# Kernel tuning notes

Measured on AMD Instinct MI355X. Metric: run time of the kernel, lower is better.

## Reference

```python
import jax, jax.numpy as jnp
import numpy as np

D_MODEL = 768
D_STATE = 16
K_CONV = 4
BATCH = 2
SEQ = 2048


def setup_inputs() -> dict:
    key = jax.random.key(0)
    ks = jax.random.split(key, 16)
    dm, ds, K = D_MODEL, D_STATE, K_CONV
    s = 0.02
    inp = {
        "x": jax.random.normal(ks[0], (BATCH, SEQ, dm), dtype=jnp.float32),
        # linear weights stored (in, out); y = x @ W + b (equivalent to torch Linear)
        "Wi": jax.random.normal(ks[1], (dm, 2 * dm), dtype=jnp.float32) * s,
        "bi": jnp.zeros((2 * dm,), jnp.float32),
        "Wconv": jax.random.normal(ks[2], (dm, K), dtype=jnp.float32) * s,
        "bconv": jnp.zeros((dm,), jnp.float32),
        "Wdt": jax.random.normal(ks[3], (dm, dm), dtype=jnp.float32) * s,
        "bdt": jnp.zeros((dm,), jnp.float32),
        "WB": jax.random.normal(ks[4], (dm, dm * ds), dtype=jnp.float32) * s,
        "bB": jnp.zeros((dm * ds,), jnp.float32),
        "WC": jax.random.normal(ks[5], (dm, dm * ds), dtype=jnp.float32) * s,
        "bC": jnp.zeros((dm * ds,), jnp.float32),
        "A_log": jnp.zeros((dm, ds), jnp.float32),  # matches nn.Parameter(torch.zeros)
        "D": jnp.ones((dm,), jnp.float32),          # matches nn.Parameter(torch.ones)
        "Wo": jax.random.normal(ks[6], (dm, dm), dtype=jnp.float32) * s,
        "bo": jnp.zeros((dm,), jnp.float32),
    }
    return inp


def _forward(x, Wi, bi, Wconv, bconv, Wdt, bdt, WB, bB, WC, bC, A_log, D, Wo, bo):
    B, L, dm = x.shape
    ds = A_log.shape[1]
    K = Wconv.shape[1]

    uv = x @ Wi + bi                        # (B, L, 2*dm)
    u, v = uv[..., :dm], uv[..., dm:]

    # causal depthwise conv1d: torch pads K-1 both sides, keeps first L outputs
    u_pad = jnp.pad(u, ((0, 0), (K - 1, 0), (0, 0)))
    u_conv = bconv + sum(u_pad[:, k:k + L, :] * Wconv[:, k] for k in range(K))

    dt = jax.nn.softplus(u_conv @ Wdt + bdt)            # (B, L, dm)
    Bt = (u_conv @ WB + bB).reshape(B, L, dm, ds)       # (B, L, dm, ds)
    Ct = (u_conv @ WC + bC).reshape(B, L, dm, ds)
    A = -jnp.exp(A_log)                                  # (dm, ds)

    def step(s, inputs):
        dt_t, u_t, B_tt, C_tt = inputs                   # (B,dm), (B,dm), (B,dm,ds), (B,dm,ds)
        dt_e = dt_t[..., None]
        s = s * jnp.exp(dt_e * A) + dt_e * B_tt * u_t[..., None]
        y = jnp.sum(C_tt * s, axis=-1) + D * u_t         # (B, dm)
        return s, y

    s0 = jnp.zeros((B, dm, ds), x.dtype)
    xs = (dt.transpose(1, 0, 2), u_conv.transpose(1, 0, 2),
          Bt.transpose(1, 0, 2, 3), Ct.transpose(1, 0, 2, 3))
    _, ys = jax.lax.scan(step, s0, xs)                   # ys: (L, B, dm)
    y = ys.transpose(1, 0, 2)

    y = y * jax.nn.sigmoid(v)
    return y @ Wo + bo


def reference(x, Wi, bi, Wconv, bconv, Wdt, bdt, WB, bB, WC, bC, A_log, D, Wo, bo):
    return _forward(x, Wi, bi, Wconv, bconv, Wdt, bdt, WB, bB, WC, bC, A_log, D, Wo, bo)
```

## Files before the change

kernel.cpp:

```cpp
#include <hip/hip_runtime.h>

#define DM 768
#define DS 16
#define SEQ 2048
#define BATCH 2
#define MROWS (BATCH*SEQ)
#define N_UV (2*DM)
#define N_BC (DM*DS)
#define NGRP (BATCH*DM/4)
#define SWAVES 16

typedef _Float16 half8 __attribute__((ext_vector_type(8)));
typedef float floatx4 __attribute__((ext_vector_type(4)));
typedef int i32x4 __attribute__((ext_vector_type(4)));
typedef unsigned short us8 __attribute__((ext_vector_type(8)));
typedef signed char c8 __attribute__((ext_vector_type(8)));

static __device__ __forceinline__ unsigned short f2h(float f) {
  _Float16 h = (_Float16)f;
  return __builtin_bit_cast(unsigned short, h);
}
static __device__ __forceinline__ float h2f(unsigned short u) {
  return (float)__builtin_bit_cast(_Float16, u);
}
static __device__ __forceinline__ float softplus_f(float x) {
  return (x > 20.f) ? x : log1pf(__expf(x));
}
static __device__ __forceinline__ void async_cp16(const void* g, void* l) {
  __builtin_amdgcn_global_load_lds(
      (const __attribute__((address_space(1))) void*)g,
      (__attribute__((address_space(3))) void*)l, 16, 0, 0);
}
static __device__ __forceinline__ float row_reduce16(float v) {
  int x;
  x = __builtin_amdgcn_update_dpp(0, __builtin_bit_cast(int, v), 0x128, 0xf, 0xf, true);
  v += __builtin_bit_cast(float, x);
  x = __builtin_amdgcn_update_dpp(0, __builtin_bit_cast(int, v), 0x124, 0xf, 0xf, true);
  v += __builtin_bit_cast(float, x);
  x = __builtin_amdgcn_update_dpp(0, __builtin_bit_cast(int, v), 0x122, 0xf, 0xf, true);
  v += __builtin_bit_cast(float, x);
  x = __builtin_amdgcn_update_dpp(0, __builtin_bit_cast(int, v), 0x121, 0xf, 0xf, true);
  v += __builtin_bit_cast(float, x);
  return v;
}

__global__ void convert_f2h(const float* __restrict__ in,
                            unsigned short* __restrict__ out, int n) {
  int i = (blockIdx.x * blockDim.x + threadIdx.x) * 4;
  if (i >= n) return;
  float4 f = *(const float4*)(in + i);
  ushort4 h;
  h.x = f2h(f.x); h.y = f2h(f.y); h.z = f2h(f.z); h.w = f2h(f.w);
  *(ushort4*)(out + i) = h;
}

__global__ void transpose_w5(const float* __restrict__ W0, const float* __restrict__ W1,
                             const float* __restrict__ W2, const float* __restrict__ W3,
                             const float* __restrict__ W4,
                             unsigned short* __restrict__ T0, unsigned short* __restrict__ T1,
                             unsigned short* __restrict__ T2, unsigned short* __restrict__ T3,
                             unsigned short* __restrict__ T4,
                             int N0, int N1, int N2, int N3, int N4) {
  const float* W; unsigned short* WT; int N;
  switch (blockIdx.z) {
    case 0: W = W0; WT = T0; N = N0; break;
    case 1: W = W1; WT = T1; N = N1; break;
    case 2: W = W2; WT = T2; N = N2; break;
    case 3: W = W3; WT = T3; N = N3; break;
    default: W = W4; WT = T4; N = N4; break;
  }
  int n0 = blockIdx.x * 32;
  if (n0 >= N) return;
  int k0 = blockIdx.y * 32;
  __shared__ float tile[32][33];
  int tx = threadIdx.x, ty = threadIdx.y;
#pragma unroll
  for (int i = 0; i < 32; i += 8)
    tile[ty + i][tx] = W[(size_t)(k0 + ty + i) * N + (n0 + tx)];
  __syncthreads();
  int kp = tx & 15, half = tx >> 4;
#pragma unroll
  for (int i = 0; i < 2; i++) {
    int nl = ty + half * 8 + i * 16;
    unsigned int pk = (unsigned int)f2h(tile[2 * kp][nl]) |
                      ((unsigned int)f2h(tile[2 * kp + 1][nl]) << 16);
    *(unsigned int*)&WT[(size_t)(n0 + nl) * DM + k0 + 2 * kp] = pk;
  }
}

__global__ void transpose_act3(const unsigned short* __restrict__ dt,
                               const unsigned short* __restrict__ uc,
                               const unsigned short* __restrict__ uv,
                               unsigned short* __restrict__ dtT,
                               unsigned short* __restrict__ ucT,
                               unsigned short* __restrict__ vT) {
  const unsigned short* src; unsigned short* dst; int ld, coff;
  switch (blockIdx.z) {
    case 0:  src = dt; dst = dtT; ld = DM;   coff = 0;  break;
    case 1:  src = uc; dst = ucT; ld = DM;   coff = 0;  break;
    default: src = uv; dst = vT;  ld = N_UV; coff = DM; break;
  }
  __shared__ unsigned short tile[32][33];
  int r0 = blockIdx.x * 32, c0 = blockIdx.y * 32;
  int tx = threadIdx.x, ty = threadIdx.y;
#pragma unroll
  for (int i = 0; i < 32; i += 8)
    tile[ty + i][tx] = src[(size_t)(r0 + ty + i) * ld + coff + c0 + tx];
  __syncthreads();
#pragma unroll
  for (int i = 0; i < 32; i += 8)
    dst[(size_t)(c0 + ty + i) * MROWS + r0 + tx] = tile[tx][ty + i];
}

__global__ __launch_bounds__(256)
void quant_rows(const unsigned short* __restrict__ in0,
                const unsigned short* __restrict__ in1,
                signed char* __restrict__ out0, signed char* __restrict__ out1,
                float* __restrict__ sc0, float* __restrict__ sc1, int R) {
  const unsigned short* in = blockIdx.y ? in1 : in0;
  signed char* out = blockIdx.y ? out1 : out0;
  float* scp = blockIdx.y ? sc1 : sc0;
  int row = blockIdx.x * 4 + (threadIdx.x >> 6);
  if (row >= R) return;
  int lane = threadIdx.x & 63;
  const us8* ch = (const us8*)(in + (size_t)row * DM);
  us8 a = ch[lane];
  us8 b = ch[64 + (lane & 31)];
  float fa[8], fb[8];
  float m = 0.f;
#pragma unroll
  for (int j = 0; j < 8; j++) { fa[j] = h2f(a[j]); m = fmaxf(m, fabsf(fa[j])); }
#pragma unroll
  for (int j = 0; j < 8; j++) fb[j] = h2f(b[j]);
  if (lane < 32) {
#pragma unroll
    for (int j = 0; j < 8; j++) m = fmaxf(m, fabsf(fb[j]));
  }
#pragma unroll
  for (int off = 32; off; off >>= 1) m = fmaxf(m, __shfl_xor(m, off));
  float inv = (m > 0.f) ? 127.f / m : 0.f;
  if (lane == 0) scp[row] = m * (1.f / 127.f);
  c8 qa, qb;
#pragma unroll
  for (int j = 0; j < 8; j++)
    qa[j] = (signed char)__float2int_rn(fminf(fmaxf(fa[j] * inv, -127.f), 127.f));
#pragma unroll
  for (int j = 0; j < 8; j++)
    qb[j] = (signed char)__float2int_rn(fminf(fmaxf(fb[j] * inv, -127.f), 127.f));
  c8* o = (c8*)(out + (size_t)row * DM);
  o[lane] = qa;
  if (lane < 32) o[64 + lane] = qb;
}

template<int ACT, int OUTH>
__global__ __launch_bounds__(256)
void gemm_f16(const unsigned short* __restrict__ A,
              const unsigned short* __restrict__ BT0,
              const unsigned short* __restrict__ BT1,
              const float* __restrict__ bias0,
              const float* __restrict__ bias1,
              void* __restrict__ Cout0,
              void* __restrict__ Cout1,
              int M, int N, int K, int TCa, int bstride, int row0) {
  const unsigned short* BT = blockIdx.z ? BT1 : BT0;
  const float* bias = blockIdx.z ? bias1 : bias0;
  void* Cout = blockIdx.z ? Cout1 : Cout0;
  __shared__ __align__(16) unsigned short As[128 * 32];
  __shared__ __align__(16) unsigned short Bs[128 * 32];
  const int m0 = blockIdx.y * 128, n0 = blockIdx.x * 128;
  const int tid = threadIdx.x;
  const int lane = tid & 63, wave = tid >> 6;
  const int wm = (wave >> 1) * 64, wn = (wave & 1) * 64;
  const int l16 = lane & 15, quad = lane >> 4;
  const int sr = tid >> 2;
  const int sc = (((tid & 3) ^ ((tid >> 3) & 3))) * 8;
  const int pch = (quad ^ ((l16 >> 1) & 3)) * 8;

  floatx4 acc[4][4] = {};

  const int mA0 = m0 + sr, mA1 = m0 + sr + 64;
  const int gA0 = (mA0 / TCa) * bstride + row0 + (mA0 % TCa);
  const int gA1 = (mA1 / TCa) * bstride + row0 + (mA1 % TCa);
  const unsigned short* Arow0 = A + (size_t)gA0 * K + sc;
  const unsigned short* Arow1 = A + (size_t)gA1 * K + sc;
  const unsigned short* Brow0 = BT + (size_t)(n0 + sr) * K + sc;
  const unsigned short* Brow1 = BT + (size_t)(n0 + sr + 64) * K + sc;
  unsigned short* ldsA0 = As + (wave * 16) * 32;
  unsigned short* ldsA1 = As + (64 + wave * 16) * 32;
  unsigned short* ldsB0 = Bs + (wave * 16) * 32;
  unsigned short* ldsB1 = Bs + (64 + wave * 16) * 32;

  for (int k0 = 0; k0 < K; k0 += 32) {
    async_cp16(Arow0 + k0, ldsA0);
    async_cp16(Arow1 + k0, ldsA1);
    async_cp16(Brow0 + k0, ldsB0);
    async_cp16(Brow1 + k0, ldsB1);
    __syncthreads();
    half8 af[4], bf[4];
#pragma unroll
    for (int i = 0; i < 4; i++) {
      af[i] = __builtin_bit_cast(half8, *(const uint4*)&As[(wm + i * 16 + l16) * 32 + pch]);
      bf[i] = __builtin_bit_cast(half8, *(const uint4*)&Bs[(wn + i * 16 + l16) * 32 + pch]);
    }
#pragma unroll
    for (int mi = 0; mi < 4; mi++)
#pragma unroll
      for (int ni = 0; ni < 4; ni++)
        acc[mi][ni] = __builtin_amdgcn_mfma_f32_16x16x32_f16(af[mi], bf[ni], acc[mi][ni], 0, 0, 0);
    __syncthreads();
  }

#pragma unroll
  for (int ni = 0; ni < 4; ni++) {
    int col = n0 + wn + ni * 16 + l16;
    float bv = bias[col];
#pragma unroll
    for (int mi = 0; mi < 4; mi++) {
#pragma unroll
      for (int r = 0; r < 4; r++) {
        int row = m0 + wm + mi * 16 + quad * 4 + r;
        float v = acc[mi][ni][r] + bv;
        if (ACT == 1) v = softplus_f(v);
        if (OUTH) ((unsigned short*)Cout)[(size_t)row * N + col] = f2h(v);
        else      ((float*)Cout)[(size_t)row * N + col] = v;
      }
    }
  }
}

__global__ __launch_bounds__(256)
void gemm_i8(const signed char* __restrict__ A,
             const signed char* __restrict__ BT0,
             const signed char* __restrict__ BT1,
             const float* __restrict__ bias0,
             const float* __restrict__ bias1,
             const float* __restrict__ sA,
             const float* __restrict__ sB0,
             const float* __restrict__ sB1,
             unsigned short* __restrict__ C0,
             unsigned short* __restrict__ C1,
             int M, int N, int K, int TCa, int bstride, int row0) {
  const signed char* BT = blockIdx.z ? BT1 : BT0;
  const float* bias = blockIdx.z ? bias1 : bias0;
  const float* sB = blockIdx.z ? sB1 : sB0;
  unsigned short* Cout = blockIdx.z ? C1 : C0;
  __shared__ __align__(16) signed char As[128 * 64];
  __shared__ __align__(16) signed char Bs[128 * 64];
  const int m0 = blockIdx.y * 128, n0 = blockIdx.x * 128;
  const int tid = threadIdx.x;
  const int lane = tid & 63, wave = tid >> 6;
  const int wm = (wave >> 1) * 64, wn = (wave & 1) * 64;
  const int l16 = lane & 15, quad = lane >> 4;
  const int sr = tid >> 2;
  const int sc = ((tid & 3) ^ ((tid >> 3) & 3)) * 16;
  const int pch = (quad ^ ((l16 >> 1) & 3)) * 16;

  i32x4 acc[4][4] = {};

  const int mA0 = m0 + sr, mA1 = m0 + sr + 64;
  const int gA0 = (mA0 / TCa) * bstride + row0 + (mA0 % TCa);
  const int gA1 = (mA1 / TCa) * bstride + row0 + (mA1 % TCa);
  const signed char* Arow0 = A + (size_t)gA0 * K + sc;
  const signed char* Arow1 = A + (size_t)gA1 * K + sc;
  const signed char* Brow0 = BT + (size_t)(n0 + sr) * K + sc;
  const signed char* Brow1 = BT + (size_t)(n0 + sr + 64) * K + sc;
  signed char* ldsA0 = As + (wave * 16) * 64;
  signed char* ldsA1 = As + (64 + wave * 16) * 64;
  signed char* ldsB0 = Bs + (wave * 16) * 64;
  signed char* ldsB1 = Bs + (64 + wave * 16) * 64;

  for (int k0 = 0; k0 < K; k0 += 64) {
    async_cp16(Arow0 + k0, ldsA0);
    async_cp16(Arow1 + k0, ldsA1);
    async_cp16(Brow0 + k0, ldsB0);
    async_cp16(Brow1 + k0, ldsB1);
    __syncthreads();
    i32x4 af[4], bf[4];
#pragma unroll
    for (int i = 0; i < 4; i++) {
      af[i] = *(const i32x4*)&As[(wm + i * 16 + l16) * 64 + pch];
      bf[i] = *(const i32x4*)&Bs[(wn + i * 16 + l16) * 64 + pch];
    }
#pragma unroll
    for (int mi = 0; mi < 4; mi++)
#pragma unroll
      for (int ni = 0; ni < 4; ni++)
        acc[mi][ni] = __builtin_amdgcn_mfma_i32_16x16x64_i8(af[mi], bf[ni], acc[mi][ni], 0, 0, 0);
    __syncthreads();
  }

  const int rowAbase = (m0 / TCa) * (bstride - TCa) + row0;
  float savs[4][4];
#pragma unroll
  for (int mi = 0; mi < 4; mi++)
#pragma unroll
    for (int r = 0; r < 4; r++)
      savs[mi][r] = sA[rowAbase + m0 + wm + mi * 16 + quad * 4 + r];

#pragma unroll
  for (int ni = 0; ni < 4; ni++) {
    int col = n0 + wn + ni * 16 + l16;
    float bv = bias[col];
    float sbv = sB[col];
#pragma unroll
    for (int mi = 0; mi < 4; mi++) {
#pragma unroll
      for (int r = 0; r < 4; r++) {
        int row = m0 + wm + mi * 16 + quad * 4 + r;
        float v = (float)acc[mi][ni][r] * (savs[mi][r] * sbv) + bv;
        Cout[(size_t)row * N + col] = f2h(v);
      }
    }
  }
}

__global__ void dwconv(const unsigned short* __restrict__ uv,
                       const float* __restrict__ Wconv,
                       const float* __restrict__ bconv,
                       unsigned short* __restrict__ uc) {
  int idx = blockIdx.x * 256 + threadIdx.x;
  int c = (idx % (DM / 2)) * 2;
  int row = idx / (DM / 2);
  int t = row & (SEQ - 1);
  float a0 = bconv[c], a1 = bconv[c + 1];
  const float* w0 = Wconv + c * 4;
  const float* w1 = Wconv + (c + 1) * 4;
#pragma unroll
  for (int k = 0; k < 4; k++) {
    int tt = t - 3 + k;
    if (tt >= 0) {
      ushort2 u2 = *(const ushort2*)&uv[(size_t)(row - 3 + k) * N_UV + c];
      a0 += h2f(u2.x) * w0[k];
      a1 += h2f(u2.y) * w1[k];
    }
  }
  ushort2 o; o.x = f2h(a0); o.y = f2h(a1);
  *(ushort2*)&uc[(size_t)row * DM + c] = o;
}

__global__ __launch_bounds__(1024)
void scan_fused(const unsigned short* __restrict__ dtT,
                const unsigned short* __restrict__ ucT,
                const unsigned short* __restrict__ vT,
                const unsigned short* __restrict__ Btc,
                const unsigned short* __restrict__ Ctc,
                const float* __restrict__ A_log,
                const float* __restrict__ Dv,
                float* __restrict__ s_state,
                unsigned short* __restrict__ yg,
                int ci, int TC) {
  const int TSUB = TC / SWAVES;
  int wid = blockIdx.x;
  int b = wid / (DM / 4);
  int c0 = (wid % (DM / 4)) * 4;
  int wave = threadIdx.x >> 6;
  int lane = threadIdx.x & 63;
  int j = lane & 15;
  int c = c0 + (lane >> 4);
  float Acj = -__expf(A_log[c0 * DS + lane]);
  float Dc = Dv[c];
  int col = c0 * DS + lane;
  int sidx = b * N_BC + col;
  float s0 = (ci == 0) ? 0.f : s_state[sidx];
  size_t tbase = (size_t)b * SEQ + (size_t)ci * TC + (size_t)wave * TSUB;
  size_t lbase = (size_t)b * TC + (size_t)wave * TSUB;
  const unsigned short* dtp = dtT + (size_t)c * MROWS + tbase;
  const unsigned short* ucp = ucT + (size_t)c * MROWS + tbase;
  const unsigned short* vp  = vT  + (size_t)c * MROWS + tbase;

  __shared__ float Ssub[SWAVES][64];
  __shared__ float Aex[SWAVES][64];

  float s = 0.f, dsum = 0.f;
  {
    us8 ndt = *(const us8*)dtp;
    us8 nuc = *(const us8*)ucp;
    float n_B[8];
#pragma unroll
    for (int i = 0; i < 8; i++)
      n_B[i] = h2f(Btc[(lbase + i) * N_BC + col]);
    for (int t0 = 0; t0 < TSUB; t0 += 8) {
      us8 cdt = ndt, cuc = nuc;
      float c_B[8];
#pragma unroll
      for (int i = 0; i < 8; i++) c_B[i] = n_B[i];
      if (t0 + 8 < TSUB) {
        ndt = *(const us8*)&dtp[t0 + 8];
        nuc = *(const us8*)&ucp[t0 + 8];
#pragma unroll
        for (int i = 0; i < 8; i++)
          n_B[i] = h2f(Btc[(lbase + t0 + 8 + i) * N_BC + col]);
      }
#pragma unroll
      for (int i = 0; i < 8; i++) {
        float dtc = h2f(cdt[i]);
        dsum += dtc;
        float a = __expf(dtc * Acj);
        s = fmaf(s, a, dtc * c_B[i] * h2f(cuc[i]));
      }
    }
  }
  Ssub[wave][lane] = s;
  Aex[wave][lane] = __expf(Acj * dsum);
  __syncthreads();

  float si = s0;
#pragma unroll
  for (int k = 0; k < SWAVES; k++) {
    if (k >= wave) break;
    si = fmaf(si, Aex[k][lane], Ssub[k][lane]);
  }
  if (wave == SWAVES - 1)
    s_state[sidx] = fmaf(si, Aex[SWAVES - 1][lane], Ssub[SWAVES - 1][lane]);

  s = si;
  {
    us8 ndt = *(const us8*)dtp;
    us8 nuc = *(const us8*)ucp;
    us8 nv  = *(const us8*)vp;
    float n_B[8], n_C[8];
#pragma unroll
    for (int i = 0; i < 8; i++) {
      size_t lr = lbase + i;
      n_B[i] = h2f(Btc[lr * N_BC + col]);
      n_C[i] = h2f(Ctc[lr * N_BC + col]);
    }
    for (int t0 = 0; t0 < TSUB; t0 += 8) {
      us8 cdt = ndt, cuc = nuc, cv = nv;
      float c_B[8], c_C[8];
#pragma unroll
      for (int i = 0; i < 8; i++) { c_B[i] = n_B[i]; c_C[i] = n_C[i]; }
      if (t0 + 8 < TSUB) {
        ndt = *(const us8*)&dtp[t0 + 8];
        nuc = *(const us8*)&ucp[t0 + 8];
        nv  = *(const us8*)&vp[t0 + 8];
#pragma unroll
        for (int i = 0; i < 8; i++) {
          size_t lr = lbase + t0 + 8 + i;
          n_B[i] = h2f(Btc[lr * N_BC + col]);
          n_C[i] = h2f(Ctc[lr * N_BC + col]);
        }
      }
#pragma unroll
      for (int i = 0; i < 8; i++) {
        float dtc = h2f(cdt[i]);
        float uci = h2f(cuc[i]);
        float a = __expf(dtc * Acj);
        s = fmaf(s, a, dtc * c_B[i] * uci);
        float yt = row_reduce16(c_C[i] * s);
        if (j == 0) {
          float y = yt + Dc * uci;
          float g = 1.f / (1.f + __expf(-h2f(cv[i])));
          yg[(tbase + t0 + i) * DM + c] = f2h(y * g);
        }
      }
    }
  }
}

extern "C" void kernel_launch(void* const* d_in, const int* in_sizes, int n_in,
                              void* d_out, int out_size, void* d_ws, size_t ws_size,
                              hipStream_t stream) {
  const float* x     = (const float*)d_in[0];
  const float* Wi    = (const float*)d_in[1];
  const float* bi    = (const float*)d_in[2];
  const float* Wconv = (const float*)d_in[3];
  const float* bconv = (const float*)d_in[4];
  const float* Wdt   = (const float*)d_in[5];
  const float* bdt   = (const float*)d_in[6];
  const float* WB    = (const float*)d_in[7];
  const float* bB    = (const float*)d_in[8];
  const float* WC    = (const float*)d_in[9];
  const float* bC    = (const float*)d_in[10];
  const float* A_log = (const float*)d_in[11];
  const float* Dv    = (const float*)d_in[12];
  const float* Wo    = (const float*)d_in[13];
  const float* bo    = (const float*)d_in[14];
  float* out = (float*)d_out;
  (void)in_sizes; (void)n_in; (void)out_size;

  auto pad = [](size_t b) { return (b + 255) & ~(size_t)255; };

  const size_t sz_xb   = pad((size_t)MROWS * DM * 2);
  const size_t sz_WiT  = pad((size_t)N_UV * DM * 2);
  const size_t sz_WdtT = pad((size_t)DM * DM * 2);
  const size_t sz_WBT  = pad((size_t)N_BC * DM * 2);
  const size_t sz_WCT  = pad((size_t)N_BC * DM * 2);
  const size_t sz_WoT  = pad((size_t)DM * DM * 2);
  const size_t sz_uvb  = pad((size_t)MROWS * N_UV * 2);
  const size_t sz_ucb  = pad((size_t)MROWS * DM * 2);
  const size_t sz_dtb  = pad((size_t)MROWS * DM * 2);
  const size_t sz_actT = pad((size_t)DM * MROWS * 2);
  const size_t sz_st   = pad((size_t)BATCH * N_BC * 4);
  const size_t sz_uc8  = pad((size_t)MROWS * DM);
  const size_t sz_w8   = pad((size_t)N_BC * DM);
  const size_t sz_sA   = pad((size_t)MROWS * 4);
  const size_t sz_sB   = pad((size_t)N_BC * 4);
  const size_t fixed = sz_xb + sz_WiT + sz_WdtT + sz_WBT + sz_WCT + sz_WoT +
                       sz_uvb + sz_ucb + sz_dtb + 3 * sz_actT + sz_st +
                       sz_uc8 + 2 * sz_w8 + sz_sA + 2 * sz_sB;

  int NC = 16;
  for (int nc : {2, 4, 8, 16}) {
    size_t need = fixed + 2 * pad((size_t)BATCH * (SEQ / nc) * N_BC * 2);
    if (need <= ws_size) { NC = nc; break; }
  }
  const int TC = SEQ / NC;
  const int MC = BATCH * TC;

  char* ws = (char*)d_ws;
  size_t off = 0;
  auto alloc = [&](size_t bytes) { char* p = ws + off; off += bytes; return p; };
  unsigned short* xb   = (unsigned short*)alloc(sz_xb);
  unsigned short* WiT  = (unsigned short*)alloc(sz_WiT);
  unsigned short* WdtT = (unsigned short*)alloc(sz_WdtT);
  unsigned short* WBT  = (unsigned short*)alloc(sz_WBT);
  unsigned short* WCT  = (unsigned short*)alloc(sz_WCT);
  unsigned short* WoT  = (unsigned short*)alloc(sz_WoT);
  unsigned short* uvb  = (unsigned short*)alloc(sz_uvb);
  unsigned short* ucb  = (unsigned short*)alloc(sz_ucb);
  unsigned short* dtb  = (unsigned short*)alloc(sz_dtb);
  unsigned short* dtT  = (unsigned short*)alloc(sz_actT);
  unsigned short* ucT  = (unsigned short*)alloc(sz_actT);
  unsigned short* vT   = (unsigned short*)alloc(sz_actT);
  float*          sst  = (float*)alloc(sz_st);
  signed char*    uc8  = (signed char*)alloc(sz_uc8);
  signed char*    WBT8 = (signed char*)alloc(sz_w8);
  signed char*    WCT8 = (signed char*)alloc(sz_w8);
  float*          sAu  = (float*)alloc(sz_sA);
  float*          sB0  = (float*)alloc(sz_sB);
  float*          sB1  = (float*)alloc(sz_sB);
  unsigned short* Btc  = (unsigned short*)alloc(pad((size_t)MC * N_BC * 2));
  unsigned short* Ctc  = (unsigned short*)alloc(pad((size_t)MC * N_BC * 2));
  unsigned short* ygb  = xb;

  convert_f2h<<<dim3(MROWS * DM / 1024), dim3(256), 0, stream>>>(x, xb, MROWS * DM);
  transpose_w5<<<dim3(N_BC / 32, DM / 32, 5), dim3(32, 8), 0, stream>>>(
      Wi, Wdt, WB, WC, Wo, WiT, WdtT, WBT, WCT, WoT, N_UV, DM, N_BC, N_BC, DM);
  quant_rows<<<dim3(N_BC / 4, 2), 256, 0, stream>>>(WBT, WCT, WBT8, WCT8,
                                                    sB0, sB1, N_BC);

  gemm_f16<0, 1><<<dim3(N_UV / 128, MROWS / 128, 1), 256, 0, stream>>>(
      xb, WiT, WiT, bi, bi, uvb, uvb, MROWS, N_UV, DM, MROWS, 0, 0);
  dwconv<<<dim3(MROWS * DM / 512), 256, 0, stream>>>(uvb, Wconv, bconv, ucb);
  quant_rows<<<dim3(MROWS / 4, 1), 256, 0, stream>>>(ucb, ucb, uc8, uc8,
                                                     sAu, sAu, MROWS);
  gemm_f16<1, 1><<<dim3(DM / 128, MROWS / 128, 1), 256, 0, stream>>>(
      ucb, WdtT, WdtT, bdt, bdt, dtb, dtb, MROWS, DM, DM, MROWS, 0, 0);
  transpose_act3<<<dim3(MROWS / 32, DM / 32, 3), dim3(32, 8), 0, stream>>>(
      dtb, ucb, uvb, dtT, ucT, vT);

  for (int ci = 0; ci < NC; ci++) {
    gemm_i8<<<dim3(N_BC / 128, MC / 128, 2), 256, 0, stream>>>(
        uc8, WBT8, WCT8, bB, bC, sAu, sB0, sB1, Btc, Ctc,
        MC, N_BC, DM, TC, SEQ, ci * TC);
    scan_fused<<<dim3(NGRP), 1024, 0, stream>>>(dtT, ucT, vT, Btc, Ctc,
                                                A_log, Dv, sst, ygb, ci, TC);
  }

  gemm_f16<0, 0><<<dim3(DM / 128, MROWS / 128, 1), 256, 0, stream>>>(
      ygb, WoT, WoT, bo, bo, out, out, MROWS, DM, DM, MROWS, 0, 0);
}
```

Baseline: 638.5 us.

## Single-pass chunked scan with register-held per-step terms and fixed chunk count

```diff
diff --git a/kernel.cpp b/kernel.cpp
--- a/kernel.cpp
+++ b/kernel.cpp
@@ -8,7 +8,8 @@
 #define N_UV (2*DM)
 #define N_BC (DM*DS)
 #define NGRP (BATCH*DM/4)
-#define SWAVES 16
+#define SWAVES 8
+#define NCFIX 8
 
 typedef _Float16 half8 __attribute__((ext_vector_type(8)));
 typedef float floatx4 __attribute__((ext_vector_type(4)));
@@ -338,7 +339,7 @@
   *(ushort2*)&uc[(size_t)row * DM + c] = o;
 }
 
-__global__ __launch_bounds__(1024)
+__global__ __launch_bounds__(512)
 void scan_fused(const unsigned short* __restrict__ dtT,
                 const unsigned short* __restrict__ ucT,
                 const unsigned short* __restrict__ vT,
@@ -348,7 +349,8 @@
                 const float* __restrict__ Dv,
                 float* __restrict__ s_state,
                 unsigned short* __restrict__ yg,
-                int ci, int TC) {
+                int ci) {
+  const int TC = SEQ / NCFIX;
   const int TSUB = TC / SWAVES;
   int wid = blockIdx.x;
   int b = wid / (DM / 4);
@@ -371,69 +373,27 @@
   __shared__ float Ssub[SWAVES][64];
   __shared__ float Aex[SWAVES][64];
 
-  float s = 0.f, dsum = 0.f;
+  float q[32], cs[32];
+  float s = 0.f, P = 1.f;
+
   {
     us8 ndt = *(const us8*)dtp;
     us8 nuc = *(const us8*)ucp;
-    float n_B[8];
-#pragma unroll
-    for (int i = 0; i < 8; i++)
+    float n_B[8], n_C[8];
+#pragma unroll
+    for (int i = 0; i < 8; i++) {
       n_B[i] = h2f(Btc[(lbase + i) * N_BC + col]);
-    for (int t0 = 0; t0 < TSUB; t0 += 8) {
+      n_C[i] = h2f(Ctc[(lbase + i) * N_BC + col]);
+    }
+#pragma unroll
+    for (int t0 = 0; t0 < 32; t0 += 8) {
       us8 cdt = ndt, cuc = nuc;
-      float c_B[8];
-#pragma unroll
-      for (int i = 0; i < 8; i++) c_B[i] = n_B[i];
-      if (t0 + 8 < TSUB) {
+      float c_B[8], c_C[8];
+#pragma unroll
+      for (int i = 0; i < 8; i++) { c_B[i] = n_B[i]; c_C[i] = n_C[i]; }
+      if (t0 + 8 < 32) {
         ndt = *(const us8*)&dtp[t0 + 8];
         nuc = *(const us8*)&ucp[t0 + 8];
-#pragma unroll
-        for (int i = 0; i < 8; i++)
-          n_B[i] = h2f(Btc[(lbase + t0 + 8 + i) * N_BC + col]);
-      }
-#pragma unroll
-      for (int i = 0; i < 8; i++) {
-        float dtc = h2f(cdt[i]);
-        dsum += dtc;
-        float a = __expf(dtc * Acj);
-        s = fmaf(s, a, dtc * c_B[i] * h2f(cuc[i]));
-      }
-    }
-  }
-  Ssub[wave][lane] = s;
-  Aex[wave][lane] = __expf(Acj * dsum);
-  __syncthreads();
-
-  float si = s0;
-#pragma unroll
-  for (int k = 0; k < SWAVES; k++) {
-    if (k >= wave) break;
-    si = fmaf(si, Aex[k][lane], Ssub[k][lane]);
-  }
-  if (wave == SWAVES - 1)
-    s_state[sidx] = fmaf(si, Aex[SWAVES - 1][lane], Ssub[SWAVES - 1][lane]);
-
-  s = si;
-  {
-    us8 ndt = *(const us8*)dtp;
-    us8 nuc = *(const us8*)ucp;
-    us8 nv  = *(const us8*)vp;
-    float n_B[8], n_C[8];
-#pragma unroll
-    for (int i = 0; i < 8; i++) {
-      size_t lr = lbase + i;
-      n_B[i] = h2f(Btc[lr * N_BC + col]);
-      n_C[i] = h2f(Ctc[lr * N_BC + col]);
-    }
-    for (int t0 = 0; t0 < TSUB; t0 += 8) {
-      us8 cdt = ndt, cuc = nuc, cv = nv;
-      float c_B[8], c_C[8];
-#pragma unroll
-      for (int i = 0; i < 8; i++) { c_B[i] = n_B[i]; c_C[i] = n_C[i]; }
-      if (t0 + 8 < TSUB) {
-        ndt = *(const us8*)&dtp[t0 + 8];
-        nuc = *(const us8*)&ucp[t0 + 8];
-        nv  = *(const us8*)&vp[t0 + 8];
 #pragma unroll
         for (int i = 0; i < 8; i++) {
           size_t lr = lbase + t0 + 8 + i;
@@ -444,15 +404,38 @@
 #pragma unroll
       for (int i = 0; i < 8; i++) {
         float dtc = h2f(cdt[i]);
-        float uci = h2f(cuc[i]);
         float a = __expf(dtc * Acj);
-        s = fmaf(s, a, dtc * c_B[i] * uci);
-        float yt = row_reduce16(c_C[i] * s);
-        if (j == 0) {
-          float y = yt + Dc * uci;
-          float g = 1.f / (1.f + __expf(-h2f(cv[i])));
-          yg[(tbase + t0 + i) * DM + c] = f2h(y * g);
-        }
+        s = fmaf(s, a, dtc * c_B[i] * h2f(cuc[i]));
+        P *= a;
+        q[t0 + i]  = c_C[i] * P;
+        cs[t0 + i] = c_C[i] * s;
+      }
+    }
+  }
+  Ssub[wave][lane] = s;
+  Aex[wave][lane] = P;
+  __syncthreads();
+
+  float si = s0;
+#pragma unroll
+  for (int k = 0; k < SWAVES; k++) {
+    if (k >= wave) break;
+    si = fmaf(si, Aex[k][lane], Ssub[k][lane]);
+  }
+  if (wave == SWAVES - 1)
+    s_state[sidx] = fmaf(si, Aex[SWAVES - 1][lane], Ssub[SWAVES - 1][lane]);
+
+#pragma unroll
+  for (int t0 = 0; t0 < 32; t0 += 8) {
+    us8 cuc = *(const us8*)&ucp[t0];
+    us8 cv  = *(const us8*)&vp[t0];
+#pragma unroll
+    for (int i = 0; i < 8; i++) {
+      float yt = row_reduce16(fmaf(q[t0 + i], si, cs[t0 + i]));
+      if (j == 0) {
+        float y = yt + Dc * h2f(cuc[i]);
+        float g = 1.f / (1.f + __expf(-h2f(cv[i])));
+        yg[(tbase + t0 + i) * DM + c] = f2h(y * g);
       }
     }
   }
@@ -496,15 +479,8 @@
   const size_t sz_w8   = pad((size_t)N_BC * DM);
   const size_t sz_sA   = pad((size_t)MROWS * 4);
   const size_t sz_sB   = pad((size_t)N_BC * 4);
-  const size_t fixed = sz_xb + sz_WiT + sz_WdtT + sz_WBT + sz_WCT + sz_WoT +
-                       sz_uvb + sz_ucb + sz_dtb + 3 * sz_actT + sz_st +
-                       sz_uc8 + 2 * sz_w8 + sz_sA + 2 * sz_sB;
-
-  int NC = 16;
-  for (int nc : {2, 4, 8, 16}) {
-    size_t need = fixed + 2 * pad((size_t)BATCH * (SEQ / nc) * N_BC * 2);
-    if (need <= ws_size) { NC = nc; break; }
-  }
+
+  const int NC = NCFIX;
   const int TC = SEQ / NC;
   const int MC = BATCH * TC;
 
@@ -554,8 +530,8 @@
     gemm_i8<<<dim3(N_BC / 128, MC / 128, 2), 256, 0, stream>>>(
         uc8, WBT8, WCT8, bB, bC, sAu, sB0, sB1, Btc, Ctc,
         MC, N_BC, DM, TC, SEQ, ci * TC);
-    scan_fused<<<dim3(NGRP), 1024, 0, stream>>>(dtT, ucT, vT, Btc, Ctc,
-                                                A_log, Dv, sst, ygb, ci, TC);
+    scan_fused<<<dim3(NGRP), 512, 0, stream>>>(dtT, ucT, vT, Btc, Ctc,
+                                               A_log, Dv, sst, ygb, ci);
   }
 
   gemm_f16<0, 0><<<dim3(DM / 128, MROWS / 128, 1), 256, 0, stream>>>(
```

After: 648.1 us. Within noise of the previous version (+1.5%).
